# Performance work log

Hardware: AMD Instinct MI355X
Metric: run time of the kernel (lower is better)

The kernel has to match this reference:

```python
import jax, jax.numpy as jnp
import numpy as np

N = 100000
E = 1600000
IN_DIM, HID, NCLS = 512, 64, 16


def setup_inputs() -> dict:
    key = jax.random.key(0)
    ks = jax.random.split(key, 6)
    x = jax.random.normal(ks[0], (N, IN_DIM), dtype=jnp.float32)
    edge_index = jax.random.randint(ks[1], (2, E), 0, N, dtype=jnp.int32)
    edge_weight = jax.random.uniform(ks[2], (E,), dtype=jnp.float32)
    W1 = jax.random.normal(ks[3], (IN_DIM, HID), dtype=jnp.float32) / np.sqrt(IN_DIM)
    b1 = jnp.zeros((HID,), dtype=jnp.float32)
    W2 = jax.random.normal(ks[4], (HID, NCLS), dtype=jnp.float32) / np.sqrt(HID)
    b2 = jnp.zeros((NCLS,), dtype=jnp.float32)
    return {"x": x, "edge_index": edge_index, "edge_weight": edge_weight,
            "W1": W1, "b1": b1, "W2": W2, "b2": b2}


def _gcn_norm(edge_index, edge_weight, num_nodes):
    # PyG GCNConv: add self-loops (weight 1), symmetric deg^-1/2 normalization.
    loop = jnp.arange(num_nodes, dtype=edge_index.dtype)
    src = jnp.concatenate([edge_index[0], loop])
    dst = jnp.concatenate([edge_index[1], loop])
    w = jnp.concatenate([edge_weight, jnp.ones((num_nodes,), edge_weight.dtype)])
    deg = jax.ops.segment_sum(w, dst, num_segments=num_nodes)  # degree at target
    dis = jnp.where(deg > 0, jax.lax.rsqrt(jnp.where(deg > 0, deg, 1.0)), 0.0)
    norm = dis[src] * w * dis[dst]
    return src, dst, norm


def _gcn_layer(x, src, dst, norm, W, b):
    h = x @ W                                   # [N, out]
    msg = h[src] * norm[:, None]                # gather + scale  [E+N, out]
    out = jax.ops.segment_sum(msg, dst, num_segments=x.shape[0])
    return out + b


def reference(x, edge_index, edge_weight, W1, b1, W2, b2):
    src, dst, norm = _gcn_norm(edge_index, edge_weight, x.shape[0])
    h = _gcn_layer(x, src, dst, norm, W1, b1)
    h = jax.nn.relu(h)
    # F.dropout in eval mode is identity (reference assumes inference).
    h = _gcn_layer(h, src, dst, norm, W2, b2)
    return jax.nn.log_softmax(h, axis=-1)
```

## Files before the change

### kernel.cpp

```cpp
#include <hip/hip_runtime.h>
#include <hip/hip_bf16.h>

#define N_NODES 100000
#define N_EDGES 1600000
#define IN_DIM 512
#define HID 64
#define NCLS 16
#define NB ((N_NODES + 1023) / 1024)

#define GEMM_BLOCKS ((N_NODES + 63) / 64)
#define PASS_BLOCKS ((N_EDGES + 255) / 256)
#define FUSED_GRID (GEMM_BLOCKS + PASS_BLOCKS)

typedef __attribute__((ext_vector_type(8))) short bf16x8;
typedef __attribute__((ext_vector_type(8))) unsigned short ushort8;
typedef __attribute__((ext_vector_type(4))) float f32x4;

static __device__ __forceinline__ unsigned short f2bf(float f) {
    union { float f; unsigned int u; } v; v.f = f;
    unsigned int u = v.u;
    unsigned int r = (u + 0x7fffu + ((u >> 16) & 1u)) >> 16;
    return (unsigned short)r;
}
static __device__ __forceinline__ float bf2f(unsigned short u) {
    union { unsigned int i; float f; } v; v.i = ((unsigned int)u) << 16; return v.f;
}
static __device__ __forceinline__ unsigned int f2bf2u(float a, float b) {
    union { __hip_bfloat162 h; unsigned int u; } cv;
    cv.h = __float22bfloat162_rn(make_float2(a, b));
    return cv.u;
}


__global__ void k_setup(int* cnt, const float* __restrict__ W1,
                        unsigned short* __restrict__ wt) {
    int t = blockIdx.x * 256 + threadIdx.x;
    if (t < N_NODES) cnt[t] = 0;
    int j = t - N_NODES;
    if (j >= 0 && j < HID * IN_DIM) {
        int n = j >> 9, k = j & 511;
        wt[j] = f2bf(W1[(size_t)k * HID + n]);
    }
}


#define LDK 72

__global__ __launch_bounds__(256) void k_fused(const int* __restrict__ dst,
                                               int* cnt, int* __restrict__ li,
                                               const float* __restrict__ x,
                                               const unsigned short* __restrict__ wt,
                                               unsigned short* __restrict__ h1s) {
    __shared__ unsigned short xs[64][LDK];
    __shared__ unsigned short ws[64][LDK];

    int b = blockIdx.x;
    int q = b / 5, r = b % 5;
    if (r != 0) {
        int pid = q * 4 + r - 1;
        int e = pid * 256 + threadIdx.x;
        if (e < N_EDGES) li[e] = atomicAdd(&cnt[dst[e]], 1);
        return;
    }
    int gid = q;
    int t = threadIdx.x;
    int row0 = gid * 64;
    int wave = t >> 6, lane = t & 63;
    int lm = lane & 15, quad = lane >> 4;

    f32x4 acc[4];
#pragma unroll
    for (int nt = 0; nt < 4; nt++) acc[nt] = (f32x4)(0.f);

    for (int k0 = 0; k0 < IN_DIM; k0 += 64) {
        __syncthreads();
        {
            int c8 = (t & 7) * 8;
#pragma unroll
            for (int h = 0; h < 2; h++) {
                int rr = (t >> 3) + h * 32;
                int gr = row0 + rr;
                if (gr >= N_NODES) gr = N_NODES - 1;
                const float* xp = x + (size_t)gr * IN_DIM + k0 + c8;
                float4 v0 = *(const float4*)xp;
                float4 v1 = *(const float4*)(xp + 4);
                union { ushort8 s; unsigned int u[4]; } pk;
                pk.u[0] = f2bf2u(v0.x, v0.y);
                pk.u[1] = f2bf2u(v0.z, v0.w);
                pk.u[2] = f2bf2u(v1.x, v1.y);
                pk.u[3] = f2bf2u(v1.z, v1.w);
                *(ushort8*)&xs[rr][c8] = pk.s;
            }
        }
        {
            int n = t >> 2, kc = (t & 3) * 16;
            const unsigned short* wp = wt + (size_t)n * IN_DIM + k0 + kc;
            *(ushort8*)&ws[n][kc]     = *(const ushort8*)wp;
            *(ushort8*)&ws[n][kc + 8] = *(const ushort8*)(wp + 8);
        }
        __syncthreads();
#pragma unroll
        for (int kk = 0; kk < 64; kk += 32) {
            bf16x8 afrag = *(bf16x8*)&xs[wave * 16 + lm][kk + quad * 8];
#pragma unroll
            for (int nt = 0; nt < 4; nt++) {
                bf16x8 bfrag = *(bf16x8*)&ws[nt * 16 + lm][kk + quad * 8];
                acc[nt] = __builtin_amdgcn_mfma_f32_16x16x32_bf16(afrag, bfrag, acc[nt], 0, 0, 0);
            }
        }
    }
#pragma unroll
    for (int i = 0; i < 4; i++) {
        int gr = row0 + wave * 16 + quad * 4 + i;
        if (gr < N_NODES) {
#pragma unroll
            for (int nt = 0; nt < 4; nt++)
                h1s[(size_t)gr * HID + nt * 16 + lm] = f2bf(acc[nt][i]);
        }
    }
}


__global__ void k_scan1(const int* __restrict__ cnt, int* ptr, int* bsum) {
    __shared__ int s[256];
    int t = threadIdx.x;
    int i0 = blockIdx.x * 1024 + t * 4;
    int c[4];
#pragma unroll
    for (int j = 0; j < 4; j++) c[j] = (i0 + j < N_NODES) ? cnt[i0 + j] : 0;
    int sum4 = c[0] + c[1] + c[2] + c[3];
    s[t] = sum4;
    __syncthreads();
    int v = sum4;
    for (int off = 1; off < 256; off <<= 1) {
        int add = (t >= off) ? s[t - off] : 0;
        __syncthreads();
        v += add;
        s[t] = v;
        __syncthreads();
    }
    int run = v - sum4;
#pragma unroll
    for (int j = 0; j < 4; j++) {
        if (i0 + j < N_NODES) ptr[i0 + j] = run;
        run += c[j];
    }
    if (t == 255) bsum[blockIdx.x] = v;
}

__global__ void k_scan2(int* bsum, int* ptr) {
    __shared__ int s[128];
    int t = threadIdx.x;
    int val = (t < NB) ? bsum[t] : 0;
    s[t] = val;
    __syncthreads();
    int v = val;
    for (int off = 1; off < 128; off <<= 1) {
        int add = (t >= off) ? s[t - off] : 0;
        __syncthreads();
        v += add;
        s[t] = v;
        __syncthreads();
    }
    if (t < NB) bsum[t] = v - val;
    if (t == 0) ptr[N_NODES] = N_EDGES;
}

__global__ void k_scan3(int* ptr, const int* __restrict__ bsum) {
    int t = threadIdx.x;
    int i0 = blockIdx.x * 1024 + t * 4;
    int add = bsum[blockIdx.x];
#pragma unroll
    for (int j = 0; j < 4; j++)
        if (i0 + j < N_NODES) ptr[i0 + j] += add;
}


__global__ void k_pass2(const int* __restrict__ src, const int* __restrict__ dst,
                        const float* __restrict__ w, const int* __restrict__ ptr,
                        const int* __restrict__ li, int2* __restrict__ csr) {
    int e = blockIdx.x * 256 + threadIdx.x;
    if (e < N_EDGES) {
        int p = ptr[dst[e]] + li[e];
        csr[p] = make_int2(src[e], __float_as_int(w[e]));
    }
}


__global__ void k_degsum(const int* __restrict__ ptr, const int2* __restrict__ csr,
                         float* __restrict__ dis) {
    int v = blockIdx.x * 256 + threadIdx.x;
    if (v < N_NODES) {
        int p0 = ptr[v], p1 = ptr[v + 1];
        float s = 1.0f;
        for (int p = p0; p < p1; p++) s += __int_as_float(csr[p].y);
        dis[v] = rsqrtf(s);
    }
}


__global__ __launch_bounds__(256) void k_agg1(const unsigned short* __restrict__ h1s,
                                              const int* __restrict__ ptr,
                                              const int2* __restrict__ csr,
                                              const float* __restrict__ dis,
                                              const float* __restrict__ b1,
                                              unsigned short* __restrict__ a1s) {
    int t = blockIdx.x * 256 + threadIdx.x;
    int v = t >> 4, c = t & 15;
    if (v >= N_NODES) return;
    int p0 = ptr[v], p1 = ptr[v + 1];

    float a0 = 0.f, a1v = 0.f, a2 = 0.f, a3 = 0.f;
    for (int base = p0; base < p1; base += 8) {
#pragma unroll
        for (int u = 0; u < 8; u++) {
            int idx = base + u;
            bool valid = idx < p1;
            int2 cw = valid ? csr[idx] : make_int2(v, 0);
            int s = cw.x;
            float wgt = __int_as_float(cw.y) * dis[s];
            ushort4 g = *(const ushort4*)&h1s[(size_t)s * HID + c * 4];
            a0 += wgt * bf2f(g.x);
            a1v += wgt * bf2f(g.y);
            a2 += wgt * bf2f(g.z);
            a3 += wgt * bf2f(g.w);
        }
    }
    float dv = dis[v], dvv = dv * dv;
    ushort4 sv = *(const ushort4*)&h1s[(size_t)v * HID + c * 4];
    float4 bv = *(const float4*)&b1[c * 4];
    float r0 = dv * a0 + dvv * bf2f(sv.x) + bv.x;
    float r1 = dv * a1v + dvv * bf2f(sv.y) + bv.y;
    float r2 = dv * a2 + dvv * bf2f(sv.z) + bv.z;
    float r3 = dv * a3 + dvv * bf2f(sv.w) + bv.w;
    ushort4 o;
    o.x = f2bf(r0 > 0.f ? r0 : 0.f);
    o.y = f2bf(r1 > 0.f ? r1 : 0.f);
    o.z = f2bf(r2 > 0.f ? r2 : 0.f);
    o.w = f2bf(r3 > 0.f ? r3 : 0.f);
    *(ushort4*)&a1s[(size_t)v * HID + c * 4] = o;
}


__global__ __launch_bounds__(256) void k_gemm2(const unsigned short* __restrict__ a1s,
                                               const float* __restrict__ W2,
                                               unsigned short* __restrict__ h2s) {
    __shared__ float ws[HID * NCLS];
    for (int i = threadIdx.x; i < HID * NCLS; i += 256) ws[i] = W2[i];
    __syncthreads();
    int t = blockIdx.x * 256 + threadIdx.x;
    int v = t >> 4, cc = t & 15;
    if (v >= N_NODES) return;
    const unsigned short* row = a1s + (size_t)v * HID;
    float acc = 0.f;
#pragma unroll
    for (int k = 0; k < HID; k += 4) {
        ushort4 av = *(const ushort4*)(row + k);
        acc = fmaf(bf2f(av.x), ws[(k + 0) * NCLS + cc], acc);
        acc = fmaf(bf2f(av.y), ws[(k + 1) * NCLS + cc], acc);
        acc = fmaf(bf2f(av.z), ws[(k + 2) * NCLS + cc], acc);
        acc = fmaf(bf2f(av.w), ws[(k + 3) * NCLS + cc], acc);
    }
    h2s[(size_t)v * NCLS + cc] = f2bf(acc);
}


__global__ __launch_bounds__(256) void k_agg2(const unsigned short* __restrict__ h2s,
                                              const int* __restrict__ ptr,
                                              const int2* __restrict__ csr,
                                              const float* __restrict__ dis,
                                              const float* __restrict__ b2,
                                              float* __restrict__ out) {
    int t = blockIdx.x * 256 + threadIdx.x;
    int v = t >> 4, c = t & 15;
    if (v >= N_NODES) return;
    int p0 = ptr[v], p1 = ptr[v + 1];

    float acc = 0.f;
    for (int base = p0; base < p1; base += 8) {
#pragma unroll
        for (int u = 0; u < 8; u++) {
            int idx = base + u;
            bool valid = idx < p1;
            int2 cw = valid ? csr[idx] : make_int2(v, 0);
            int s = cw.x;
            float wgt = __int_as_float(cw.y) * dis[s];
            acc += wgt * bf2f(h2s[(size_t)s * NCLS + c]);
        }
    }
    float dv = dis[v], dvv = dv * dv;
    float z = dv * acc + dvv * bf2f(h2s[(size_t)v * NCLS + c]) + b2[c];

    float mx = z;
#pragma unroll
    for (int off = 8; off >= 1; off >>= 1) mx = fmaxf(mx, __shfl_xor(mx, off, 16));
    float e = expf(z - mx);
    float s = e;
#pragma unroll
    for (int off = 8; off >= 1; off >>= 1) s += __shfl_xor(s, off, 16);
    out[(size_t)v * NCLS + c] = z - mx - logf(s);
}


extern "C" void kernel_launch(void* const* d_in, const int* in_sizes, int n_in,
                              void* d_out, int out_size, void* d_ws, size_t ws_size,
                              hipStream_t stream) {
    const float* x  = (const float*)d_in[0];
    const int*   ei = (const int*)d_in[1];
    const float* w  = (const float*)d_in[2];
    const float* W1 = (const float*)d_in[3];
    const float* b1 = (const float*)d_in[4];
    const float* W2 = (const float*)d_in[5];
    const float* b2 = (const float*)d_in[6];
    const int* src = ei;
    const int* dst = ei + N_EDGES;

    char* wsb = (char*)d_ws;
    size_t off = 0;
    auto alloc = [&](size_t bytes) {
        void* p = wsb + off;
        off += (bytes + 255) & ~(size_t)255;
        return p;
    };
    int*   cnt   = (int*)  alloc((size_t)N_NODES * 4);
    int*   li    = (int*)  alloc((size_t)N_EDGES * 4);
    int*   ptr   = (int*)  alloc((size_t)(N_NODES + 1) * 4);
    int*   bsum  = (int*)  alloc((size_t)NB * 4);
    int2*  csr   = (int2*) alloc((size_t)N_EDGES * 8);
    float* dis   = (float*)alloc((size_t)N_NODES * 4);
    unsigned short* h1s = (unsigned short*)alloc((size_t)N_NODES * HID * 2);
    unsigned short* a1s = (unsigned short*)alloc((size_t)N_NODES * HID * 2);
    unsigned short* h2s = (unsigned short*)alloc((size_t)N_NODES * NCLS * 2);
    unsigned short* wt  = (unsigned short*)alloc((size_t)HID * IN_DIM * 2);

    float* outp = (float*)d_out;

    k_setup  <<<(N_NODES + HID * IN_DIM + 255) / 256, 256, 0, stream>>>(cnt, W1, wt);
    k_fused  <<<FUSED_GRID, 256, 0, stream>>>(dst, cnt, li, x, wt, h1s);
    k_scan1  <<<NB, 256, 0, stream>>>(cnt, ptr, bsum);
    k_scan2  <<<1, 128, 0, stream>>>(bsum, ptr);
    k_scan3  <<<NB, 256, 0, stream>>>(ptr, bsum);
    k_pass2  <<<PASS_BLOCKS, 256, 0, stream>>>(src, dst, w, ptr, li, csr);
    k_degsum <<<(N_NODES + 255) / 256, 256, 0, stream>>>(ptr, csr, dis);
    k_agg1   <<<(N_NODES * 16 + 255) / 256, 256, 0, stream>>>(h1s, ptr, csr, dis, b1, a1s);
    k_gemm2  <<<(N_NODES * 16 + 255) / 256, 256, 0, stream>>>(a1s, W2, h2s);
    k_agg2   <<<(N_NODES * 16 + 255) / 256, 256, 0, stream>>>(h2s, ptr, csr, dis, b2, outp);
}
```

Before: 491.9 us.

## Fuse second GEMM into layer-1 aggregation, merge scan kernels, nontemporal x loads

```diff
diff --git a/kernel.cpp b/kernel.cpp
--- a/kernel.cpp
+++ b/kernel.cpp
@@ -81,9 +81,9 @@
                 int rr = (t >> 3) + h * 32;
                 int gr = row0 + rr;
                 if (gr >= N_NODES) gr = N_NODES - 1;
-                const float* xp = x + (size_t)gr * IN_DIM + k0 + c8;
-                float4 v0 = *(const float4*)xp;
-                float4 v1 = *(const float4*)(xp + 4);
+                const f32x4* xp = (const f32x4*)(x + (size_t)gr * IN_DIM + k0 + c8);
+                f32x4 v0 = __builtin_nontemporal_load(xp);
+                f32x4 v1 = __builtin_nontemporal_load(xp + 1);
                 union { ushort8 s; unsigned int u[4]; } pk;
                 pk.u[0] = f2bf2u(v0.x, v0.y);
                 pk.u[1] = f2bf2u(v0.z, v0.w);
@@ -148,31 +148,39 @@
     if (t == 255) bsum[blockIdx.x] = v;
 }
 
-__global__ void k_scan2(int* bsum, int* ptr) {
+
+__global__ void k_scan3(int* ptr, const int* __restrict__ bsum) {
     __shared__ int s[128];
     int t = threadIdx.x;
-    int val = (t < NB) ? bsum[t] : 0;
-    s[t] = val;
+    int val = 0;
+    if (t < 128) {
+        val = (t < NB) ? bsum[t] : 0;
+        s[t] = val;
+    }
     __syncthreads();
-    int v = val;
-    for (int off = 1; off < 128; off <<= 1) {
-        int add = (t >= off) ? s[t - off] : 0;
-        __syncthreads();
-        v += add;
+    if (t < 128) {
+        int v = val;
+        for (int off = 1; off < 128; off <<= 1) {
+            int add = (t >= off) ? s[t - off] : 0;
+            __syncthreads();
+            v += add;
+            s[t] = v;
+            __syncthreads();
+        }
+        v -= val;
+        __syncthreads();
         s[t] = v;
-        __syncthreads();
-    }
-    if (t < NB) bsum[t] = v - val;
-    if (t == 0) ptr[N_NODES] = N_EDGES;
-}
-
-__global__ void k_scan3(int* ptr, const int* __restrict__ bsum) {
-    int t = threadIdx.x;
+    } else {
+        for (int off = 1; off < 128; off <<= 1) { __syncthreads(); __syncthreads(); }
+        __syncthreads();
+    }
+    __syncthreads();
+    int add = s[blockIdx.x];
     int i0 = blockIdx.x * 1024 + t * 4;
-    int add = bsum[blockIdx.x];
 #pragma unroll
     for (int j = 0; j < 4; j++)
         if (i0 + j < N_NODES) ptr[i0 + j] += add;
+    if (blockIdx.x == 0 && t == 0) ptr[N_NODES] = N_EDGES;
 }
 
 
@@ -204,7 +212,15 @@
                                               const int2* __restrict__ csr,
                                               const float* __restrict__ dis,
                                               const float* __restrict__ b1,
-                                              unsigned short* __restrict__ a1s) {
+                                              const float* __restrict__ W2,
+                                              unsigned short* __restrict__ h2s) {
+    __shared__ float w2t[NCLS * 68];
+    for (int i = threadIdx.x; i < HID * NCLS; i += 256) {
+        int k = i >> 4, cc = i & 15;
+        w2t[cc * 68 + k] = W2[i];
+    }
+    __syncthreads();
+
     int t = blockIdx.x * 256 + threadIdx.x;
     int v = t >> 4, c = t & 15;
     if (v >= N_NODES) return;
@@ -233,35 +249,27 @@
     float r1 = dv * a1v + dvv * bf2f(sv.y) + bv.y;
     float r2 = dv * a2 + dvv * bf2f(sv.z) + bv.z;
     float r3 = dv * a3 + dvv * bf2f(sv.w) + bv.w;
-    ushort4 o;
-    o.x = f2bf(r0 > 0.f ? r0 : 0.f);
-    o.y = f2bf(r1 > 0.f ? r1 : 0.f);
-    o.z = f2bf(r2 > 0.f ? r2 : 0.f);
-    o.w = f2bf(r3 > 0.f ? r3 : 0.f);
-    *(ushort4*)&a1s[(size_t)v * HID + c * 4] = o;
-}
-
-
-__global__ __launch_bounds__(256) void k_gemm2(const unsigned short* __restrict__ a1s,
-                                               const float* __restrict__ W2,
-                                               unsigned short* __restrict__ h2s) {
-    __shared__ float ws[HID * NCLS];
-    for (int i = threadIdx.x; i < HID * NCLS; i += 256) ws[i] = W2[i];
-    __syncthreads();
-    int t = blockIdx.x * 256 + threadIdx.x;
-    int v = t >> 4, cc = t & 15;
-    if (v >= N_NODES) return;
-    const unsigned short* row = a1s + (size_t)v * HID;
-    float acc = 0.f;
-#pragma unroll
-    for (int k = 0; k < HID; k += 4) {
-        ushort4 av = *(const ushort4*)(row + k);
-        acc = fmaf(bf2f(av.x), ws[(k + 0) * NCLS + cc], acc);
-        acc = fmaf(bf2f(av.y), ws[(k + 1) * NCLS + cc], acc);
-        acc = fmaf(bf2f(av.z), ws[(k + 2) * NCLS + cc], acc);
-        acc = fmaf(bf2f(av.w), ws[(k + 3) * NCLS + cc], acc);
-    }
-    h2s[(size_t)v * NCLS + cc] = f2bf(acc);
+    r0 = r0 > 0.f ? r0 : 0.f;
+    r1 = r1 > 0.f ? r1 : 0.f;
+    r2 = r2 > 0.f ? r2 : 0.f;
+    r3 = r3 > 0.f ? r3 : 0.f;
+
+    float partial[NCLS];
+#pragma unroll
+    for (int cc = 0; cc < NCLS; cc++) {
+        const float* wp = &w2t[cc * 68 + 4 * c];
+        partial[cc] = r0 * wp[0] + r1 * wp[1] + r2 * wp[2] + r3 * wp[3];
+    }
+#pragma unroll
+    for (int m = 1; m <= 8; m <<= 1)
+#pragma unroll
+        for (int cc = 0; cc < NCLS; cc++)
+            partial[cc] += __shfl_xor(partial[cc], m, 16);
+
+    float sel = partial[0];
+#pragma unroll
+    for (int cc = 1; cc < NCLS; cc++) sel = (c == cc) ? partial[cc] : sel;
+    h2s[(size_t)v * NCLS + c] = f2bf(sel);
 }
 
 
@@ -329,7 +337,6 @@
     int2*  csr   = (int2*) alloc((size_t)N_EDGES * 8);
     float* dis   = (float*)alloc((size_t)N_NODES * 4);
     unsigned short* h1s = (unsigned short*)alloc((size_t)N_NODES * HID * 2);
-    unsigned short* a1s = (unsigned short*)alloc((size_t)N_NODES * HID * 2);
     unsigned short* h2s = (unsigned short*)alloc((size_t)N_NODES * NCLS * 2);
     unsigned short* wt  = (unsigned short*)alloc((size_t)HID * IN_DIM * 2);
 
@@ -338,11 +345,9 @@
     k_setup  <<<(N_NODES + HID * IN_DIM + 255) / 256, 256, 0, stream>>>(cnt, W1, wt);
     k_fused  <<<FUSED_GRID, 256, 0, stream>>>(dst, cnt, li, x, wt, h1s);
     k_scan1  <<<NB, 256, 0, stream>>>(cnt, ptr, bsum);
-    k_scan2  <<<1, 128, 0, stream>>>(bsum, ptr);
     k_scan3  <<<NB, 256, 0, stream>>>(ptr, bsum);
     k_pass2  <<<PASS_BLOCKS, 256, 0, stream>>>(src, dst, w, ptr, li, csr);
     k_degsum <<<(N_NODES + 255) / 256, 256, 0, stream>>>(ptr, csr, dis);
-    k_agg1   <<<(N_NODES * 16 + 255) / 256, 256, 0, stream>>>(h1s, ptr, csr, dis, b1, a1s);
-    k_gemm2  <<<(N_NODES * 16 + 255) / 256, 256, 0, stream>>>(a1s, W2, h2s);
+    k_agg1   <<<(N_NODES * 16 + 255) / 256, 256, 0, stream>>>(h1s, ptr, csr, dis, b1, W2, h2s);
     k_agg2   <<<(N_NODES * 16 + 255) / 256, 256, 0, stream>>>(h2s, ptr, csr, dis, b2, outp);
 }
```

Result: slower. 501.7 us (+2.0%).
